# Kernel tuning notes

Measured on AMD Instinct MI355X. Metric: run time of the kernel, lower is better.

Reference implementation:

```python
import jax, jax.numpy as jnp
import numpy as np

N = 25000
E = 400000
MUL0 = 64   # multiplicity of 0e node irreps
MUL1 = 32   # multiplicity of 1o node irreps
NUM_BASIS = 10
FC_HIDDEN = 100
WEIGHT_NUMEL = 2 * MUL0 + 3 * MUL1  # 224: per-edge tp weights for the 5 uvu paths
MID_S = MUL0 + MUL1       # 96 mid scalar channels
MID_V = MUL0 + 2 * MUL1   # 128 mid vector channels
NUM_NEIGHBORS = 16.0


def setup_inputs() -> dict:
    key = jax.random.key(0)
    ks = jax.random.split(key, 16)
    inp = {
        'node_scalars': jax.random.normal(ks[0], (N, MUL0), jnp.float32),
        'node_vectors': jax.random.normal(ks[1], (N, MUL1, 3), jnp.float32),
        'node_attr': jnp.ones((N, 1), jnp.float32),
        'edge_src': jax.random.randint(ks[2], (E,), 0, N, jnp.int32),
        'edge_dst': jax.random.randint(ks[3], (E,), 0, N, jnp.int32),
        'edge_attr': jax.random.normal(ks[4], (E, 4), jnp.float32),
        'edge_scalars': jax.random.normal(ks[5], (E, NUM_BASIS), jnp.float32),
        # FullyConnectedNet: [10, 100, weight_numel], silu on hidden
        'W_fc1': jax.random.normal(ks[6], (NUM_BASIS, FC_HIDDEN), jnp.float32) / np.sqrt(NUM_BASIS),
        'W_fc2': jax.random.normal(ks[7], (FC_HIDDEN, WEIGHT_NUMEL), jnp.float32) / np.sqrt(FC_HIDDEN),
        # FullyConnectedTensorProduct with 0e attr == per-irrep linear mixing
        'W_sc_s': jax.random.normal(ks[8], (MUL0, MUL0), jnp.float32) / np.sqrt(MUL0),
        'W_sc_v': jax.random.normal(ks[9], (MUL1, MUL1), jnp.float32) / np.sqrt(MUL1),
        'W_l1_s': jax.random.normal(ks[10], (MUL0, MUL0), jnp.float32) / np.sqrt(MUL0),
        'W_l1_v': jax.random.normal(ks[11], (MUL1, MUL1), jnp.float32) / np.sqrt(MUL1),
        'W_l2_s': jax.random.normal(ks[12], (MID_S, MUL0), jnp.float32) / np.sqrt(MID_S),
        'W_l2_v': jax.random.normal(ks[13], (MID_V, MUL1), jnp.float32) / np.sqrt(MID_V),
        'W_l3': jax.random.normal(ks[14], (MID_S, 1), jnp.float32) / np.sqrt(MID_S),
    }
    return inp


def reference(node_scalars, node_vectors, node_attr, edge_src, edge_dst, edge_attr,
              edge_scalars, W_fc1, W_fc2, W_sc_s, W_sc_v, W_l1_s, W_l1_v,
              W_l2_s, W_l2_v, W_l3):
    n = node_scalars.shape[0]
    # --- edge-weight FC net: silu hidden, linear out -> per-edge tp weights ---
    w = jax.nn.silu(edge_scalars @ W_fc1) @ W_fc2  # [E, 224]
    w_00, w_01 = w[:, :MUL0], w[:, MUL0:2 * MUL0]                  # paths from 0e input
    w_10 = w[:, 2 * MUL0:2 * MUL0 + MUL1]                          # 1o x 0e -> 1o
    w_11s = w[:, 2 * MUL0 + MUL1:2 * MUL0 + 2 * MUL1]              # 1o x 1o -> 0e
    w_11v = w[:, 2 * MUL0 + 2 * MUL1:]                             # 1o x 1o -> 1o

    attr = node_attr  # [N,1] (0e attr => scalar multiplier)
    # self-connection and lin1 (per-irrep linear * attr)
    sc_s = (node_scalars @ W_sc_s) * attr
    sc_v = jnp.einsum('nuc,uv->nvc', node_vectors, W_sc_v) * attr[:, :, None]
    f_s = (node_scalars @ W_l1_s) * attr
    f_v = jnp.einsum('nuc,uv->nvc', node_vectors, W_l1_v) * attr[:, :, None]

    # --- gather source node features per edge ---
    s = f_s[edge_src]          # [E, MUL0]
    v = f_v[edge_src]          # [E, MUL1, 3]
    y0 = edge_attr[:, :1]      # l=0 sh
    y1 = edge_attr[:, 1:4]     # l=1 sh

    # --- weighted tensor product (uvu), CG-contracted paths ---
    mid_s = jnp.concatenate([
        w_00 * s * y0,                                              # 0e x 0e -> 0e
        w_11s * jnp.einsum('euc,ec->eu', v, y1) / jnp.sqrt(3.0),    # 1o x 1o -> 0e
    ], axis=1)                                                      # [E, 96]
    mid_v = jnp.concatenate([
        w_01[:, :, None] * s[:, :, None] * y1[:, None, :],          # 0e x 1o -> 1o
        w_10[:, :, None] * v * y0[:, :, None],                      # 1o x 0e -> 1o
        w_11v[:, :, None] * jnp.cross(v, y1[:, None, :]) / jnp.sqrt(2.0),  # 1o x 1o -> 1o
    ], axis=1)                                                      # [E, 128, 3]

    # --- scatter-add aggregation into destination nodes ---
    inv = 1.0 / jnp.sqrt(NUM_NEIGHBORS)
    agg_s = jax.ops.segment_sum(mid_s, edge_dst, num_segments=n) * inv
    agg_v = jax.ops.segment_sum(mid_v, edge_dst, num_segments=n) * inv

    # --- output linears and gated residual mix ---
    conv_s = (agg_s @ W_l2_s) * attr
    conv_v = jnp.einsum('nuc,uv->nvc', agg_v, W_l2_v) * attr[:, :, None]
    angle = 0.1 * (agg_s @ W_l3) * attr  # [N,1]
    cos, sin = jnp.cos(angle), jnp.sin(angle)  # sc output_mask is all-ones here
    out_s = cos * sc_s + sin * conv_s
    out_v = cos[:, :, None] * sc_v + sin[:, :, None] * conv_v
    return jnp.concatenate([out_s, out_v.reshape(n, -1)], axis=1)  # [N, 64+96]
```

## Files before the change

kernel.cpp:

```cpp
#include <hip/hip_runtime.h>

#define MUL0 64
#define MUL1 32
#define NBASIS 10
#define FCH 100
#define WNUMEL 224
#define MIDS 96
#define MIDV 128
#define EG 4

#define OFF_W1   0
#define OFF_W2   1000
#define OFF_WSCS 23400
#define OFF_WSCV 27496
#define OFF_WL1S 28520
#define OFF_WL1V 32616
#define OFF_WL2S 33640
#define OFF_WL2V 39784
#define OFF_WL3  43880
#define OFF_WEND 43976
#define OFF_FLAG 43980
#define OFF_W1FRAG 44032
#define OFF_W2FRAG 45824
#define OFF_DYN  60160

#define W1FRAG_N (112 * 32)
#define W2FRAG_N (4 * 224 * 32)

typedef __attribute__((ext_vector_type(8))) short short8;
typedef __attribute__((ext_vector_type(4))) float f32x4;

__device__ __forceinline__ float bf2f(unsigned short h) {
    unsigned int u = ((unsigned int)h) << 16;
    float f; __builtin_memcpy(&f, &u, 4); return f;
}
__device__ __forceinline__ unsigned short f2bf(float f) {
    unsigned int u; __builtin_memcpy(&u, &f, 4);
    u += 0x7fffu + ((u >> 16) & 1u);
    return (unsigned short)(u >> 16);
}
__device__ __forceinline__ float fast_silu(float x) {
    return x * __builtin_amdgcn_rcpf(1.0f + __expf(-x));
}
template<bool BF>
__device__ __forceinline__ float ldf(const void* p, size_t i) {
    if constexpr (BF) return bf2f(((const unsigned short*)p)[i]);
    else              return ((const float*)p)[i];
}
template<bool BF>
__device__ __forceinline__ void stf(void* p, size_t i, float v) {
    if constexpr (BF) ((unsigned short*)p)[i] = f2bf(v);
    else              ((float*)p)[i] = v;
}
template<bool BF>
__device__ __forceinline__ f32x4 ld4(const void* p, size_t i) {
    if constexpr (BF) {
        ushort4 h = *(const ushort4*)((const unsigned short*)p + i);
        return (f32x4){bf2f(h.x), bf2f(h.y), bf2f(h.z), bf2f(h.w)};
    } else {
        return *(const f32x4*)((const float*)p + i);
    }
}
__device__ __forceinline__ int wave_incl_scan(int v) {
    int lane = threadIdx.x & 63;
    #pragma unroll
    for (int d = 1; d < 64; d <<= 1) {
        int t = __shfl_up(v, d, 64);
        if (lane >= d) v += t;
    }
    return v;
}

template<bool BF>
__device__ __forceinline__ void node_pre_body(
    const void* __restrict__ ns, const void* __restrict__ nv,
    const void* __restrict__ attr,
    const void* __restrict__ Wl1s, const void* __restrict__ Wl1v,
    float* __restrict__ f_s, float* __restrict__ f_v, int i, int Nn)
{
    int stotal = Nn * MUL0;
    if (i < stotal) {
        int n = i >> 6, j = i & 63;
        float a = 0.f;
        #pragma unroll
        for (int u = 0; u < MUL0; u++)
            a = fmaf(ldf<BF>(ns, (size_t)n * MUL0 + u), ldf<BF>(Wl1s, u * MUL0 + j), a);
        f_s[i] = a * ldf<BF>(attr, n);
    } else {
        int m = i - stotal;
        if (m >= Nn * MUL1 * 3) return;
        int n = m / 96; int idx = m - n * 96;
        int vi = idx / 3; int c = idx - vi * 3;
        float a = 0.f;
        #pragma unroll
        for (int u = 0; u < MUL1; u++)
            a = fmaf(ldf<BF>(nv, (size_t)n * 96 + u * 3 + c), ldf<BF>(Wl1v, u * MUL1 + vi), a);
        f_v[m] = a * ldf<BF>(attr, n);
    }
}

__global__ __launch_bounds__(256) void k_prep(
    const void* __restrict__ ns, const void* __restrict__ nv,
    const void* __restrict__ attr,
    const void* __restrict__ a0, const void* __restrict__ a1,
    const void* __restrict__ a2, const void* __restrict__ a3,
    const void* __restrict__ a4, const void* __restrict__ a5,
    const void* __restrict__ a6, const void* __restrict__ a7,
    const void* __restrict__ a8,
    float* __restrict__ wsf,
    unsigned short* __restrict__ w1frag, unsigned short* __restrict__ w2frag,
    int* __restrict__ cnt, int* __restrict__ flag,
    float* __restrict__ f_s, float* __restrict__ f_v, int Nn)
{
    const bool bf = (((const unsigned int*)attr)[0] == 0x3F803F80u);
    int i = blockIdx.x * 256 + threadIdx.x;
    if (i == 0) *flag = bf ? 1 : 0;

    const int npre = Nn * 160;
    if (i < npre) {
        if (bf) node_pre_body<true >(ns, nv, attr, a4, a5, f_s, f_v, i, Nn);
        else    node_pre_body<false>(ns, nv, attr, a4, a5, f_s, f_v, i, Nn);
        return;
    }
    int m = i - npre;
    if (m < OFF_WEND) {
        const void* p; int off = m;
        if      (m < OFF_W2)   { p = a0; }
        else if (m < OFF_WSCS) { p = a1; off = m - OFF_W2; }
        else if (m < OFF_WSCV) { p = a2; off = m - OFF_WSCS; }
        else if (m < OFF_WL1S) { p = a3; off = m - OFF_WSCV; }
        else if (m < OFF_WL1V) { p = a4; off = m - OFF_WL1S; }
        else if (m < OFF_WL2S) { p = a5; off = m - OFF_WL1V; }
        else if (m < OFF_WL2V) { p = a6; off = m - OFF_WL2S; }
        else if (m < OFF_WL3)  { p = a7; off = m - OFF_WL2V; }
        else                   { p = a8; off = m - OFF_WL3; }
        wsf[m] = bf ? ldf<true>(p, off) : ldf<false>(p, off);
        return;
    }
    m -= OFF_WEND;
    if (m < W1FRAG_N) {
        int col = m >> 5, k = m & 31;
        float v = 0.f;
        if (col < FCH && k < NBASIS)
            v = bf ? ldf<true>(a0, k * FCH + col) : ldf<false>(a0, k * FCH + col);
        w1frag[m] = f2bf(v);
        return;
    }
    m -= W1FRAG_N;
    if (m < W2FRAG_N) {
        int q = m / (224 * 32); int r = m - q * 224 * 32;
        int n = r >> 5; int kk = r & 31;
        int k = q * 32 + kk;
        float v = 0.f;
        if (k < FCH)
            v = bf ? ldf<true>(a1, k * WNUMEL + n) : ldf<false>(a1, k * WNUMEL + n);
        w2frag[m] = f2bf(v);
        return;
    }
    m -= W2FRAG_N;
    if (m < Nn) cnt[m] = 0;
}

__global__ __launch_bounds__(256) void k_hist(
    const int* __restrict__ edst, int* __restrict__ cnt, int Ecnt)
{
    int e = blockIdx.x * 256 + threadIdx.x;
    if (e < Ecnt) atomicAdd(&cnt[edst[e]], 1);
}

__global__ __launch_bounds__(256) void k_scan_blk(
    const int* __restrict__ cnt, int* __restrict__ row_part,
    int* __restrict__ blk_sum, int Nn)
{
    __shared__ int ws4[4];
    int tid = threadIdx.x, lane = tid & 63, wid = tid >> 6;
    int i = blockIdx.x * 256 + tid;
    int v = (i < Nn) ? cnt[i] : 0;
    int incl = wave_incl_scan(v);
    if (lane == 63) ws4[wid] = incl;
    __syncthreads();
    int off = 0;
    #pragma unroll
    for (int w2 = 0; w2 < 4; w2++) off += (w2 < wid) ? ws4[w2] : 0;
    if (i < Nn) row_part[i] = off + incl - v;
    if (tid == 0) blk_sum[blockIdx.x] = ws4[0] + ws4[1] + ws4[2] + ws4[3];
}

__global__ __launch_bounds__(256) void k_scan_top(
    const int* __restrict__ blk_sum, int* __restrict__ blk_off,
    int* __restrict__ row_start, int NB, int Nn)
{
    __shared__ int ws4[4];
    int tid = threadIdx.x, lane = tid & 63, wid = tid >> 6;
    int v = (tid < NB) ? blk_sum[tid] : 0;
    int incl = wave_incl_scan(v);
    if (lane == 63) ws4[wid] = incl;
    __syncthreads();
    int off = 0;
    #pragma unroll
    for (int w2 = 0; w2 < 4; w2++) off += (w2 < wid) ? ws4[w2] : 0;
    if (tid < NB) blk_off[tid] = off + incl - v;
    if (tid == 0) row_start[Nn] = ws4[0] + ws4[1] + ws4[2] + ws4[3];
}

__global__ __launch_bounds__(256) void k_rowfix(
    const int* __restrict__ row_part, const int* __restrict__ blk_off,
    int* __restrict__ row_start, int* __restrict__ cur, int Nn)
{
    int i = blockIdx.x * 256 + threadIdx.x;
    if (i < Nn) { row_start[i] = blk_off[i >> 8] + row_part[i]; cur[i] = 0; }
}

__global__ __launch_bounds__(1024) void k_scan1(
    const int* __restrict__ cnt, int* __restrict__ row_start,
    int* __restrict__ cur, int Nn)
{
    __shared__ int wsum[16];
    __shared__ int s_off, s_tot;
    int tid = threadIdx.x, lane = tid & 63, wid = tid >> 6;
    if (tid == 0) s_off = 0;
    __syncthreads();
    for (int base = 0; base < Nn; base += 1024) {
        int i = base + tid;
        int v = (i < Nn) ? cnt[i] : 0;
        int incl = wave_incl_scan(v);
        if (lane == 63) wsum[wid] = incl;
        __syncthreads();
        if (wid == 0) {
            int wv = (lane < 16) ? wsum[lane] : 0;
            int wincl = wave_incl_scan(wv);
            if (lane < 16) wsum[lane] = wincl - wv;
            if (lane == 15) s_tot = wincl;
        }
        __syncthreads();
        int excl = s_off + wsum[wid] + incl - v;
        if (i < Nn) { row_start[i] = excl; cur[i] = 0; }
        __syncthreads();
        if (tid == 0) s_off += s_tot;
        __syncthreads();
    }
    if (threadIdx.x == 0) row_start[Nn] = s_off;
}

__global__ __launch_bounds__(256) void k_place(
    const int* __restrict__ edst, const int* __restrict__ esrc,
    const void* __restrict__ eattr,
    const int* __restrict__ row_start, int* __restrict__ cur,
    int* __restrict__ perm, int* __restrict__ srcs, float* __restrict__ y4,
    int Ecnt, const int* __restrict__ flag, int extras)
{
    int e = blockIdx.x * 256 + threadIdx.x;
    if (e >= Ecnt) return;
    int d = edst[e];
    int pos = row_start[d] + atomicAdd(&cur[d], 1);
    perm[pos] = e;
    if (extras) {
        srcs[pos] = esrc[e];
        float4 yv;
        if (*flag) {
            const unsigned short* ap = (const unsigned short*)eattr + (size_t)e * 4;
            yv = make_float4(bf2f(ap[0]), bf2f(ap[1]), bf2f(ap[2]), bf2f(ap[3]));
        } else {
            const float* ap = (const float*)eattr + (size_t)e * 4;
            yv = make_float4(ap[0], ap[1], ap[2], ap[3]);
        }
        ((float4*)y4)[pos] = yv;
    }
}

#define HFC_STRIDE 136
#define WS_STRIDE 232

__global__ __launch_bounds__(256) void k_fc(
    const void* __restrict__ escal, const int* __restrict__ perm,
    const unsigned short* __restrict__ w1frag, const unsigned short* __restrict__ w2frag,
    unsigned short* __restrict__ wbuf, int Ecnt, const int* __restrict__ flag)
{
    __shared__ __align__(16) unsigned short h_lds[64 * HFC_STRIDE];
    __shared__ __align__(16) unsigned short w_stage[64 * WS_STRIDE];
    const int tid  = threadIdx.x;
    const int lane = tid & 63;
    const int wave = tid >> 6;
    const int nl   = lane & 15;
    const int quad = lane >> 4;
    const int tb   = blockIdx.x * 64;

    for (int i = tid; i < 64 * 16; i += 256) {
        int row = i >> 4;
        h_lds[row * HFC_STRIDE + 112 + (i & 15)] = 0;
    }

    int eidx = tb + 16 * wave + nl;
    if (eidx >= Ecnt) eidx = Ecnt - 1;
    const int e = perm[eidx];
    short8 a = {0, 0, 0, 0, 0, 0, 0, 0};
    if (*flag) {
        const unsigned int* p = (const unsigned int*)((const unsigned short*)escal + (size_t)e * NBASIS);
        if (quad == 0) {
            unsigned int d0 = p[0], d1 = p[1], d2 = p[2], d3 = p[3];
            a = (short8){(short)d0, (short)(d0 >> 16), (short)d1, (short)(d1 >> 16),
                         (short)d2, (short)(d2 >> 16), (short)d3, (short)(d3 >> 16)};
        } else if (quad == 1) {
            unsigned int d4 = p[4];
            a = (short8){(short)d4, (short)(d4 >> 16), 0, 0, 0, 0, 0, 0};
        }
    } else {
        const float* p = (const float*)escal + (size_t)e * NBASIS;
        if (quad == 0) {
            a = (short8){(short)f2bf(p[0]), (short)f2bf(p[1]), (short)f2bf(p[2]), (short)f2bf(p[3]),
                         (short)f2bf(p[4]), (short)f2bf(p[5]), (short)f2bf(p[6]), (short)f2bf(p[7])};
        } else if (quad == 1) {
            a = (short8){(short)f2bf(p[8]), (short)f2bf(p[9]), 0, 0, 0, 0, 0, 0};
        }
    }

    {
        f32x4 hacc[7];
        #pragma unroll
        for (int t = 0; t < 7; t++) {
            short8 b = *(const short8*)&w1frag[(16 * t + nl) * 32 + quad * 8];
            hacc[t] = __builtin_amdgcn_mfma_f32_16x16x32_bf16(
                a, b, (f32x4){0.f, 0.f, 0.f, 0.f}, 0, 0, 0);
        }
        #pragma unroll
        for (int t = 0; t < 7; t++) {
            #pragma unroll
            for (int r = 0; r < 4; r++)
                h_lds[(16 * wave + quad * 4 + r) * HFC_STRIDE + 16 * t + nl] =
                    f2bf(fast_silu(hacc[t][r]));
        }
    }
    __syncthreads();

    #pragma unroll 2
    for (int t = 0; t < 14; t++) {
        f32x4 c = {0.f, 0.f, 0.f, 0.f};
        #pragma unroll
        for (int q = 0; q < 4; q++) {
            short8 av = *(const short8*)&h_lds[(16 * wave + nl) * HFC_STRIDE + q * 32 + quad * 8];
            short8 b = *(const short8*)&w2frag[((q * 224) + 16 * t + nl) * 32 + quad * 8];
            c = __builtin_amdgcn_mfma_f32_16x16x32_bf16(av, b, c, 0, 0, 0);
        }
        #pragma unroll
        for (int r = 0; r < 4; r++)
            w_stage[(16 * wave + quad * 4 + r) * WS_STRIDE + 16 * t + nl] = f2bf(c[r]);
    }
    __syncthreads();

    {
        unsigned short* wt = wbuf + (size_t)tb * WNUMEL;
        #pragma unroll
        for (int g = 0; g < 7; g++) {
            int m = g * 256 + tid;
            int row = m / 28, c8 = m - row * 28;
            uint4 v = *(const uint4*)&w_stage[row * WS_STRIDE + c8 * 8];
            *(uint4*)&wt[(size_t)m * 8] = v;
        }
    }
}

#define AGG_BODY(IDX, S)                                                     \
  {                                                                          \
    const int idx_ = (IDX);                                                  \
    const int srcn = srcs[idx_];                                             \
    const float4 y = ((const float4*)y4)[idx_];                              \
    const unsigned short* wrow = wbuf + (size_t)idx_ * WNUMEL;               \
    const float* fsr = f_s + (size_t)srcn * 64;                              \
    const float* fvr = f_v + (size_t)srcn * 96;                              \
    float fs_l = fsr[lane];                                                  \
    float v0 = fvr[lane2 * 3 + 0];                                           \
    float v1 = fvr[lane2 * 3 + 1];                                           \
    float v2 = fvr[lane2 * 3 + 2];                                           \
    float w00 = bf2f(wrow[lane]);                                            \
    float w01 = bf2f(wrow[64 + lane]);                                       \
    float wh  = bf2f(wrow[128 + lane]);                                      \
    float wx  = bf2f(wrow[160 + lane]);                                      \
    const float y0 = y.x, y1x = y.y, y1y = y.z, y1z = y.w;                   \
    acc0##S = fmaf(w00 * fs_l, y0 * k14, acc0##S);                           \
    float dot_ = v0 * y1x + v1 * y1y + v2 * y1z;                             \
    acc1##S = fmaf(wh * dot_, k13, acc1##S);                                 \
    float t1_ = w01 * fs_l * k14;                                            \
    accS0##S = fmaf(t1_, y1x, accS0##S);                                     \
    accS1##S = fmaf(t1_, y1y, accS1##S);                                     \
    accS2##S = fmaf(t1_, y1z, accS2##S);                                     \
    float cx_ = v1 * y1z - v2 * y1y;                                         \
    float cy_ = v2 * y1x - v0 * y1z;                                         \
    float cz_ = v0 * y1y - v1 * y1x;                                         \
    float e0_ = hi ? cx_ : v0;                                               \
    float e1_ = hi ? cy_ : v1;                                               \
    float e2_ = hi ? cz_ : v2;                                               \
    float tv_ = hi ? (wx * k12) : (wh * (y0 * k14));                         \
    accV0##S = fmaf(e0_, tv_, accV0##S);                                     \
    accV1##S = fmaf(e1_, tv_, accV1##S);                                     \
    accV2##S = fmaf(e2_, tv_, accV2##S);                                     \
  }

__global__ __launch_bounds__(256) void k_agg(
    const unsigned short* __restrict__ wbuf,
    const int* __restrict__ srcs, const float* __restrict__ y4,
    const int* __restrict__ row_start,
    const float* __restrict__ f_s, const float* __restrict__ f_v,
    const float* __restrict__ Wl3, const void* __restrict__ attr,
    float* __restrict__ agg_s, float* __restrict__ aggv,
    float* __restrict__ cosb, float* __restrict__ sinb,
    int Nn, const int* __restrict__ flag)
{
    const int tid  = threadIdx.x;
    const int lane = tid & 63;
    const int wave = tid >> 6;
    const int node = blockIdx.x * EG + wave;
    if (node >= Nn) return;

    const int lane2 = lane & 31;
    const bool hi = (lane >= 32);

    const int dlo = row_start[node];
    const int dhi = row_start[node + 1];
    const int mid = dlo + ((dhi - dlo) >> 1);

    const float k14 = 0.25f;
    const float k13 = 0.25f * 0.57735026918962576451f;
    const float k12 = 0.25f * 0.70710678118654752440f;

    float acc0A = 0.f, acc1A = 0.f, accS0A = 0.f, accS1A = 0.f, accS2A = 0.f;
    float accV0A = 0.f, accV1A = 0.f, accV2A = 0.f;
    float acc0B = 0.f, acc1B = 0.f, accS0B = 0.f, accS1B = 0.f, accS2B = 0.f;
    float accV0B = 0.f, accV1B = 0.f, accV2B = 0.f;

    int iA = dlo, iB = mid;
    for (; iA < mid; ++iA, ++iB) {
        AGG_BODY(iA, A);
        AGG_BODY(iB, B);
    }
    for (; iB < dhi; ++iB) {
        AGG_BODY(iB, B);
    }

    const float acc0  = acc0A + acc0B;
    const float acc1  = acc1A + acc1B;
    const float accS0 = accS0A + accS0B;
    const float accS1 = accS1A + accS1B;
    const float accS2 = accS2A + accS2B;
    const float accV0 = accV0A + accV0B;
    const float accV1 = accV1A + accV1B;
    const float accV2 = accV2A + accV2B;

    {
        float* as = agg_s + (size_t)node * MIDS;
        float* av = aggv  + (size_t)node * 384;
        as[lane] = acc0;
        if (hi) as[64 + lane2] = acc1;

        av[0 * 128 + lane] = accS0;
        av[1 * 128 + lane] = accS1;
        av[2 * 128 + lane] = accS2;
        const int vrow = hi ? (96 + lane2) : (64 + lane);
        av[0 * 128 + vrow] = accV0;
        av[1 * 128 + vrow] = accV1;
        av[2 * 128 + vrow] = accV2;

        float avv = acc0 * Wl3[lane];
        if (hi) avv = fmaf(acc1, Wl3[64 + lane2], avv);
        #pragma unroll
        for (int d = 1; d < 64; d <<= 1) avv += __shfl_xor(avv, d);
        if (lane == 0) {
            float at = (*flag) ? ldf<true>(attr, node) : ldf<false>(attr, node);
            float aa = 0.1f * avv * at;
            cosb[node] = __cosf(aa);
            sinb[node] = __sinf(aa);
        }
    }
}

#define WT_STRIDE 164

template<bool BF>
__device__ __forceinline__ void final_s_body(
    const float* __restrict__ agg_s, const void* __restrict__ ns,
    const float* __restrict__ cosb, const float* __restrict__ sinb,
    const void* __restrict__ attr, void* __restrict__ out,
    int Nn, const float* Wt, int lane, int nb)
{
    float acc_sc[8], acc_l2[8];
    int nidx[8];
    #pragma unroll
    for (int r = 0; r < 8; r++) {
        acc_sc[r] = 0.f; acc_l2[r] = 0.f;
        int n = nb + r; nidx[r] = (n < Nn) ? n : (Nn - 1);
    }
    #pragma unroll 2
    for (int t = 0; t < 16; t++) {
        f32x4 wv = *(const f32x4*)&Wt[lane * WT_STRIDE + 4 * t];
        #pragma unroll
        for (int r = 0; r < 8; r++) {
            f32x4 x = ld4<BF>(ns, (size_t)nidx[r] * 64 + 4 * t);
            acc_sc[r] = fmaf(x[0], wv[0], acc_sc[r]);
            acc_sc[r] = fmaf(x[1], wv[1], acc_sc[r]);
            acc_sc[r] = fmaf(x[2], wv[2], acc_sc[r]);
            acc_sc[r] = fmaf(x[3], wv[3], acc_sc[r]);
        }
    }
    #pragma unroll 2
    for (int t = 0; t < 24; t++) {
        f32x4 wv = *(const f32x4*)&Wt[lane * WT_STRIDE + 64 + 4 * t];
        #pragma unroll
        for (int r = 0; r < 8; r++) {
            f32x4 x = *(const f32x4*)(agg_s + (size_t)nidx[r] * 96 + 4 * t);
            acc_l2[r] = fmaf(x[0], wv[0], acc_l2[r]);
            acc_l2[r] = fmaf(x[1], wv[1], acc_l2[r]);
            acc_l2[r] = fmaf(x[2], wv[2], acc_l2[r]);
            acc_l2[r] = fmaf(x[3], wv[3], acc_l2[r]);
        }
    }
    #pragma unroll
    for (int r = 0; r < 8; r++) {
        int n = nb + r;
        if (n < Nn) {
            float cv = cosb[n], sv = sinb[n];
            float at = ldf<BF>(attr, n);
            stf<BF>(out, (size_t)n * 160 + lane, at * (cv * acc_sc[r] + sv * acc_l2[r]));
        }
    }
}

__global__ __launch_bounds__(256) void k_final_s(
    const float* __restrict__ agg_s, const void* __restrict__ ns,
    const float* __restrict__ Wscs, const float* __restrict__ Wl2s,
    const float* __restrict__ cosb, const float* __restrict__ sinb,
    const void* __restrict__ attr, void* __restrict__ out,
    int Nn, const int* __restrict__ flag)
{
    __shared__ float Wt[64 * WT_STRIDE];
    const int tid = threadIdx.x;
    for (int i = tid; i < 160 * 64; i += 256) {
        int u = i >> 6, j = i & 63;
        float w = (u < 64) ? Wscs[u * 64 + j] : Wl2s[(u - 64) * 64 + j];
        Wt[j * WT_STRIDE + u] = w;
    }
    __syncthreads();

    const int lane = tid & 63;
    const int wave = __builtin_amdgcn_readfirstlane(tid >> 6);
    const int nb   = (blockIdx.x * 4 + wave) * 8;
    if (nb >= Nn) return;
    if (*flag) final_s_body<true >(agg_s, ns, cosb, sinb, attr, out, Nn, Wt, lane, nb);
    else       final_s_body<false>(agg_s, ns, cosb, sinb, attr, out, Nn, Wt, lane, nb);
}

template<bool BF>
__device__ __forceinline__ void final_v_body(
    const float* __restrict__ aggv, const void* __restrict__ nv,
    const float* __restrict__ cosb, const float* __restrict__ sinb,
    const void* __restrict__ attr, void* __restrict__ out,
    int Nn, const float* Wt, int lane, int ub)
{
    const int vi   = lane & 31;
    const int grp  = lane >> 5;
    const int NU   = 3 * Nn;
    float acc_sc[8], acc_l2[8];
    int gidx[8], nn_[8], cc_[8];
    #pragma unroll
    for (int r = 0; r < 8; r++) {
        acc_sc[r] = 0.f; acc_l2[r] = 0.f;
        int g = ub + grp * 8 + r;
        if (g > NU - 1) g = NU - 1;
        gidx[r] = g;
        nn_[r] = (int)((unsigned)g / 3u);
        cc_[r] = g - 3 * nn_[r];
    }
    #pragma unroll 2
    for (int t = 0; t < 8; t++) {
        f32x4 wv = *(const f32x4*)&Wt[vi * WT_STRIDE + 4 * t];
        #pragma unroll
        for (int r = 0; r < 8; r++) {
            size_t b = (size_t)nn_[r] * 96 + (size_t)(4 * t) * 3 + cc_[r];
            float x0 = ldf<BF>(nv, b);
            float x1 = ldf<BF>(nv, b + 3);
            float x2 = ldf<BF>(nv, b + 6);
            float x3 = ldf<BF>(nv, b + 9);
            acc_sc[r] = fmaf(x0, wv[0], acc_sc[r]);
            acc_sc[r] = fmaf(x1, wv[1], acc_sc[r]);
            acc_sc[r] = fmaf(x2, wv[2], acc_sc[r]);
            acc_sc[r] = fmaf(x3, wv[3], acc_sc[r]);
        }
    }
    #pragma unroll 2
    for (int t = 0; t < 32; t++) {
        f32x4 wv = *(const f32x4*)&Wt[vi * WT_STRIDE + 32 + 4 * t];
        #pragma unroll
        for (int r = 0; r < 8; r++) {
            f32x4 x = *(const f32x4*)(aggv + (size_t)gidx[r] * 128 + 4 * t);
            acc_l2[r] = fmaf(x[0], wv[0], acc_l2[r]);
            acc_l2[r] = fmaf(x[1], wv[1], acc_l2[r]);
            acc_l2[r] = fmaf(x[2], wv[2], acc_l2[r]);
            acc_l2[r] = fmaf(x[3], wv[3], acc_l2[r]);
        }
    }
    #pragma unroll
    for (int r = 0; r < 8; r++) {
        int g = ub + grp * 8 + r;
        if (g < NU) {
            int n = nn_[r], c = cc_[r];
            float cv = cosb[n], sv = sinb[n];
            float at = ldf<BF>(attr, n);
            stf<BF>(out, (size_t)n * 160 + 64 + vi * 3 + c,
                    at * (cv * acc_sc[r] + sv * acc_l2[r]));
        }
    }
}

__global__ __launch_bounds__(256) void k_final_v(
    const float* __restrict__ aggv, const void* __restrict__ nv,
    const float* __restrict__ Wscv, const float* __restrict__ Wl2v,
    const float* __restrict__ cosb, const float* __restrict__ sinb,
    const void* __restrict__ attr, void* __restrict__ out,
    int Nn, const int* __restrict__ flag)
{
    __shared__ float Wt[32 * WT_STRIDE];
    const int tid = threadIdx.x;
    for (int i = tid; i < 160 * 32; i += 256) {
        int u = i >> 5, j = i & 31;
        float w = (u < 32) ? Wscv[u * 32 + j] : Wl2v[(u - 32) * 32 + j];
        Wt[j * WT_STRIDE + u] = w;
    }
    __syncthreads();

    const int lane = tid & 63;
    const int wave = __builtin_amdgcn_readfirstlane(tid >> 6);
    const int ub   = (blockIdx.x * 4 + wave) * 16;
    if (ub >= 3 * Nn) return;
    if (*flag) final_v_body<true >(aggv, nv, cosb, sinb, attr, out, Nn, Wt, lane, ub);
    else       final_v_body<false>(aggv, nv, cosb, sinb, attr, out, Nn, Wt, lane, ub);
}

#define ES_STRIDE 40
#define H_STRIDE 136
#define WL_STRIDE 225

__global__ __launch_bounds__(256) void k_edge_mfma(
    const void* __restrict__ escal, const void* __restrict__ eattr,
    const void* __restrict__ attr,
    const int* __restrict__ esrc,
    const int* __restrict__ row_start, const int* __restrict__ perm,
    const unsigned short* __restrict__ w1frag, const unsigned short* __restrict__ w2frag,
    const float* __restrict__ Wl3,
    const float* __restrict__ f_s, const float* __restrict__ f_v,
    float* __restrict__ agg_s, float* __restrict__ agg_v,
    float* __restrict__ cosb, float* __restrict__ sinb,
    int Nn, const int* __restrict__ flag)
{
    __shared__ __align__(16) unsigned short es_lds[64 * ES_STRIDE];
    __shared__ __align__(16) unsigned short h_lds[64 * H_STRIDE];
    __shared__ __align__(16) unsigned short w_lds[64 * WL_STRIDE];
    __shared__ float y_lds[64][4];
    __shared__ int   src_lds[64];

    const int tid  = threadIdx.x;
    const int lane = tid & 63;
    const int wave = tid >> 6;
    const int nl   = lane & 15;
    const int quad = lane >> 4;
    const int gbase = blockIdx.x * EG;
    const bool isbf = (*flag != 0);

    for (int i = tid; i < 64 * 22; i += 256) {
        int row = i / 22, k = 10 + (i - row * 22);
        es_lds[row * ES_STRIDE + k] = 0;
    }
    for (int i = tid; i < 64 * 16; i += 256) {
        int row = i >> 4, k = 112 + (i & 15);
        h_lds[row * H_STRIDE + k] = 0;
    }

    const int lane2 = lane & 31;
    const int u0 = lane / 3,  c0 = lane - 3 * u0;
    const int pB = 64 + lane;
    const int uB = pB / 3,    cB = pB - 3 * uB;
    const int p2 = 128 + lane;
    const int u2 = p2 / 3,    c2 = p2 - 3 * u2;
    const int pH = 64 + lane2;
    const int uH = pH / 3,    cH = pH - 3 * uH;
    const bool half = (lane < 32);

    const int node = gbase + wave;
    const int dlo = (node < Nn) ? row_start[node] : 0;
    const int dhi = (node < Nn) ? row_start[node + 1] : 0;

    float acc[9];
    #pragma unroll
    for (int s = 0; s < 9; s++) acc[s] = 0.f;

    const int gend    = (gbase + EG < Nn) ? (gbase + EG) : Nn;
    const int e_start = row_start[gbase];
    const int e_end   = row_start[gend];

    for (int tb = e_start; tb < e_end; tb += 64) {
        const int tcnt = (e_end - tb < 64) ? (e_end - tb) : 64;
        __syncthreads();

        {
            int i = tid & 63, part = tid >> 6;
            if (i < tcnt && part < 2) {
                int e = perm[tb + i];
                if (part == 0) {
                    unsigned int* dstp = (unsigned int*)&es_lds[i * ES_STRIDE];
                    if (isbf) {
                        const unsigned int* srcp =
                            (const unsigned int*)((const unsigned short*)escal + (size_t)e * NBASIS);
                        #pragma unroll
                        for (int t2 = 0; t2 < 5; t2++) dstp[t2] = srcp[t2];
                    } else {
                        const float* srcp = (const float*)escal + (size_t)e * NBASIS;
                        #pragma unroll
                        for (int t2 = 0; t2 < 5; t2++) {
                            unsigned int lo = f2bf(srcp[2 * t2]);
                            unsigned int hi = f2bf(srcp[2 * t2 + 1]);
                            dstp[t2] = lo | (hi << 16);
                        }
                    }
                } else {
                    src_lds[i] = esrc[e];
                    if (isbf) {
                        const unsigned short* ap = (const unsigned short*)eattr + (size_t)e * 4;
                        #pragma unroll
                        for (int t2 = 0; t2 < 4; t2++) y_lds[i][t2] = bf2f(ap[t2]);
                    } else {
                        const float* ap = (const float*)eattr + (size_t)e * 4;
                        #pragma unroll
                        for (int t2 = 0; t2 < 4; t2++) y_lds[i][t2] = ap[t2];
                    }
                }
            }
        }
        __syncthreads();

        {
            short8 a = *(const short8*)&es_lds[(16 * wave + nl) * ES_STRIDE + quad * 8];
            f32x4 hacc[7];
            #pragma unroll
            for (int t = 0; t < 7; t++) {
                short8 b = *(const short8*)&w1frag[(16 * t + nl) * 32 + quad * 8];
                hacc[t] = __builtin_amdgcn_mfma_f32_16x16x32_bf16(
                    a, b, (f32x4){0.f, 0.f, 0.f, 0.f}, 0, 0, 0);
            }
            #pragma unroll
            for (int t = 0; t < 7; t++) {
                #pragma unroll
                for (int r = 0; r < 4; r++)
                    h_lds[(16 * wave + quad * 4 + r) * H_STRIDE + 16 * t + nl] =
                        f2bf(fast_silu(hacc[t][r]));
            }
        }
        __syncthreads();

        #pragma unroll 2
        for (int t = 0; t < 14; t++) {
            f32x4 c = {0.f, 0.f, 0.f, 0.f};
            #pragma unroll
            for (int q = 0; q < 4; q++) {
                short8 a = *(const short8*)&h_lds[(16 * wave + nl) * H_STRIDE + q * 32 + quad * 8];
                short8 b = *(const short8*)&w2frag[((q * 224) + 16 * t + nl) * 32 + quad * 8];
                c = __builtin_amdgcn_mfma_f32_16x16x32_bf16(a, b, c, 0, 0, 0);
            }
            #pragma unroll
            for (int r = 0; r < 4; r++)
                w_lds[(16 * wave + quad * 4 + r) * WL_STRIDE + 16 * t + nl] = f2bf(c[r]);
        }
        __syncthreads();

        {
            int lo = dlo > tb ? dlo : tb;
            int hi = dhi < tb + tcnt ? dhi : tb + tcnt;
            for (int idx = lo; idx < hi; idx++) {
                const int i = idx - tb;
                const int srcn = src_lds[i];
                const float y0  = y_lds[i][0];
                const float y1x = y_lds[i][1];
                const float y1y = y_lds[i][2];
                const float y1z = y_lds[i][3];
                const float* fsr = f_s + (size_t)srcn * 64;
                const float* fvr = f_v + (size_t)srcn * 96;
                const unsigned short* wrow = &w_lds[i * WL_STRIDE];

                float fs_l  = fsr[lane];
                float fs_u0 = fsr[u0];
                float fs_uB = fsr[uB];
                float fs_u2 = fsr[u2];
                float fvA0 = fvr[lane2 * 3], fvA1 = fvr[lane2 * 3 + 1], fvA2 = fvr[lane2 * 3 + 2];
                float fvB0 = fvr[u0 * 3],    fvB1 = fvr[u0 * 3 + 1],    fvB2 = fvr[u0 * 3 + 2];
                float fvH0 = fvr[uH * 3],    fvH1 = fvr[uH * 3 + 1],    fvH2 = fvr[uH * 3 + 2];

                float y1c0 = (c0 == 0) ? y1x : (c0 == 1) ? y1y : y1z;
                float y1cB = (cB == 0) ? y1x : (cB == 1) ? y1y : y1z;
                float y1c2 = (c2 == 0) ? y1x : (c2 == 1) ? y1y : y1z;

                float w_s0 = bf2f(wrow[lane]);
                float w_s1 = bf2f(wrow[160 + lane2]);
                float w_s2 = bf2f(wrow[64 + u0]);
                float w_s3 = bf2f(wrow[64 + uB]);
                float w_s4 = bf2f(wrow[64 + u2]);
                float w_s5 = bf2f(wrow[128 + u0]);
                float w_s6 = bf2f(wrow[128 + uH]);
                float w_s7 = bf2f(wrow[192 + u0]);
                float w_s8 = bf2f(wrow[192 + uH]);

                const float k14 = 0.25f;
                const float k13 = 0.25f * 0.57735026918962576451f;
                const float k12 = 0.25f * 0.70710678118654752440f;

                acc[0] = fmaf(w_s0 * fs_l, y0 * k14, acc[0]);
                {
                    float dot = fvA0 * y1x + fvA1 * y1y + fvA2 * y1z;
                    acc[1] = fmaf(w_s1 * dot, k13, acc[1]);
                }
                acc[2] = fmaf(w_s2 * fs_u0, k14 * y1c0, acc[2]);
                acc[3] = fmaf(w_s3 * fs_uB, k14 * y1cB, acc[3]);
                acc[4] = fmaf(w_s4 * fs_u2, k14 * y1c2, acc[4]);
                {
                    float e5 = (c0 == 0) ? fvB0 : (c0 == 1) ? fvB1 : fvB2;
                    float e6 = (cH == 0) ? fvH0 : (cH == 1) ? fvH1 : fvH2;
                    acc[5] = fmaf(w_s5 * e5, k14 * y0, acc[5]);
                    acc[6] = fmaf(w_s6 * e6, k14 * y0, acc[6]);
                }
                {
                    float cr7 = (c0 == 0) ? (fvB1 * y1z - fvB2 * y1y)
                              : (c0 == 1) ? (fvB2 * y1x - fvB0 * y1z)
                                          : (fvB0 * y1y - fvB1 * y1x);
                    float cr8 = (cH == 0) ? (fvH1 * y1z - fvH2 * y1y)
                              : (cH == 1) ? (fvH2 * y1x - fvH0 * y1z)
                                          : (fvH0 * y1y - fvH1 * y1x);
                    acc[7] = fmaf(w_s7 * cr7, k12, acc[7]);
                    acc[8] = fmaf(w_s8 * cr8, k12, acc[8]);
                }
            }
        }
    }

    if (node < Nn) {
        float* as = agg_s + (size_t)node * MIDS;
        float* av = agg_v + (size_t)node * (MIDV * 3);
        as[lane] = acc[0];
        if (half) as[64 + lane] = acc[1];
        av[lane]       = acc[2];
        av[64 + lane]  = acc[3];
        av[128 + lane] = acc[4];
        av[192 + lane] = acc[5];
        if (half) av[256 + lane] = acc[6];
        av[288 + lane] = acc[7];
        if (half) av[352 + lane] = acc[8];

        float avv = acc[0] * Wl3[lane];
        if (half) avv = fmaf(acc[1], Wl3[64 + lane], avv);
        #pragma unroll
        for (int d = 1; d < 64; d <<= 1) avv += __shfl_xor(avv, d);
        if (lane == 0) {
            float at = isbf ? ldf<true>(attr, node) : ldf<false>(attr, node);
            float a = 0.1f * avv * at;
            cosb[node] = __cosf(a);
            sinb[node] = __sinf(a);
        }
    }
}

template<bool BF>
__device__ __forceinline__ void final_body(
    const void* __restrict__ ns, const void* __restrict__ nv,
    const void* __restrict__ attr,
    const float* __restrict__ Wscs, const float* __restrict__ Wscv,
    const float* __restrict__ Wl2s, const float* __restrict__ Wl2v,
    const float* __restrict__ agg_s, const float* __restrict__ agg_v,
    const float* __restrict__ cosb, const float* __restrict__ sinb,
    void* __restrict__ out, int Nn)
{
    int i = blockIdx.x * 256 + threadIdx.x;
    int stotal = Nn * MUL0;
    if (i < stotal) {
        int n = i >> 6, j = i & 63;
        const float* ar = agg_s + (size_t)n * MIDS;
        float a1 = 0.f, a2 = 0.f;
        #pragma unroll
        for (int u = 0; u < MUL0; u++)
            a1 = fmaf(ldf<BF>(ns, (size_t)n * MUL0 + u), Wscs[u * MUL0 + j], a1);
        #pragma unroll
        for (int u = 0; u < MIDS; u++) a2 = fmaf(ar[u], Wl2s[u * MUL0 + j], a2);
        float o = ldf<BF>(attr, n) * (cosb[n] * a1 + sinb[n] * a2);
        stf<BF>(out, (size_t)n * 160 + j, o);
    } else {
        int m = i - stotal;
        if (m >= Nn * 96) return;
        int n = m / 96; int idx = m - n * 96;
        int vi = idx / 3; int c = idx - vi * 3;
        const float* ar = agg_v + (size_t)n * (MIDV * 3);
        float a1 = 0.f, a2 = 0.f;
        #pragma unroll
        for (int u = 0; u < MUL1; u++)
            a1 = fmaf(ldf<BF>(nv, (size_t)n * 96 + u * 3 + c), Wscv[u * MUL1 + vi], a1);
        #pragma unroll
        for (int u = 0; u < MIDV; u++) a2 = fmaf(ar[u * 3 + c], Wl2v[u * MUL1 + vi], a2);
        float o = ldf<BF>(attr, n) * (cosb[n] * a1 + sinb[n] * a2);
        stf<BF>(out, (size_t)n * 160 + 64 + idx, o);
    }
}
__global__ __launch_bounds__(256) void k_final(
    const void* ns, const void* nv, const void* attr,
    const float* Wscs, const float* Wscv,
    const float* Wl2s, const float* Wl2v,
    const float* agg_s, const float* agg_v,
    const float* cosb, const float* sinb,
    void* out, int Nn, const int* flag)
{
    if (*flag) final_body<true >(ns, nv, attr, Wscs, Wscv, Wl2s, Wl2v, agg_s, agg_v, cosb, sinb, out, Nn);
    else       final_body<false>(ns, nv, attr, Wscs, Wscv, Wl2s, Wl2v, agg_s, agg_v, cosb, sinb, out, Nn);
}

extern "C" void kernel_launch(void* const* d_in, const int* in_sizes, int n_in,
                              void* d_out, int out_size, void* d_ws, size_t ws_size,
                              hipStream_t stream)
{
    const void* ns    = d_in[0];
    const void* nv    = d_in[1];
    const void* attr  = d_in[2];
    const int*  esrc  = (const int*)d_in[3];
    const int*  edst  = (const int*)d_in[4];
    const void* eattr = d_in[5];
    const void* escal = d_in[6];

    const int Nn   = in_sizes[2];
    const int Ecnt = in_sizes[3];

    float* ws = (float*)d_ws;
    int* flag = (int*)(ws + OFF_FLAG);
    unsigned short* w1frag = (unsigned short*)(ws + OFF_W1FRAG);
    unsigned short* w2frag = (unsigned short*)(ws + OFF_W2FRAG);

    size_t o = OFF_DYN;
    const size_t OFF_FS   = o; o += (size_t)Nn * 64;
    const size_t OFF_FV   = o; o += (size_t)Nn * 96;
    const size_t OFF_AGGS = o; o += (size_t)Nn * 96;
    const size_t OFF_AGGV = o; o += (size_t)Nn * 384;
    const size_t OFF_COS  = o; o += Nn;
    const size_t OFF_SIN  = o; o += Nn;
    const size_t OFF_CNT  = o; o += Nn;
    const size_t OFF_ROW  = o; o += Nn + 1;
    const size_t OFF_CUR  = o; o += Nn;
    const size_t OFF_RPART= o; o += Nn;
    const size_t OFF_BSUM = o; o += 256;
    const size_t OFF_BOFF = o; o += 256;
    const size_t OFF_PERM = o; o += Ecnt;
    const size_t OFF_SRCS = o; o += Ecnt;
    o = (o + 3) & ~(size_t)3;
    const size_t OFF_Y4   = o; o += (size_t)Ecnt * 4;
    o = (o + 15) & ~(size_t)15;
    const size_t OFF_WBUF = o;
    const int tiles = (Ecnt + 63) / 64;
    o += (size_t)tiles * 64 * 112;
    const size_t need_bytes = o * sizeof(float);

    int* cnt       = (int*)(ws + OFF_CNT);
    int* row_start = (int*)(ws + OFF_ROW);
    int* cur       = (int*)(ws + OFF_CUR);
    int* row_part  = (int*)(ws + OFF_RPART);
    int* blk_sum   = (int*)(ws + OFF_BSUM);
    int* blk_off   = (int*)(ws + OFF_BOFF);
    int* perm      = (int*)(ws + OFF_PERM);
    int* srcs      = (int*)(ws + OFF_SRCS);
    float* y4      = ws + OFF_Y4;
    unsigned short* wbuf = (unsigned short*)(ws + OFF_WBUF);

    const int NB = (Nn + 255) / 256;
    const bool split = (ws_size >= need_bytes) && (NB <= 256);

    const int prep_work = Nn * 160 + OFF_WEND + W1FRAG_N + W2FRAG_N + Nn;
    k_prep<<<(prep_work + 255) / 256, 256, 0, stream>>>(
        ns, nv, attr,
        d_in[7], d_in[8], d_in[9], d_in[10], d_in[11], d_in[12],
        d_in[13], d_in[14], d_in[15],
        ws, w1frag, w2frag, cnt, flag,
        ws + OFF_FS, ws + OFF_FV, Nn);

    k_hist<<<(Ecnt + 255) / 256, 256, 0, stream>>>(edst, cnt, Ecnt);

    if (split) {
        k_scan_blk<<<NB, 256, 0, stream>>>(cnt, row_part, blk_sum, Nn);
        k_scan_top<<<1, 256, 0, stream>>>(blk_sum, blk_off, row_start, NB, Nn);
        k_rowfix<<<NB, 256, 0, stream>>>(row_part, blk_off, row_start, cur, Nn);
        k_place<<<(Ecnt + 255) / 256, 256, 0, stream>>>(
            edst, esrc, eattr, row_start, cur, perm, srcs, y4, Ecnt, flag, 1);

        k_fc<<<tiles, 256, 0, stream>>>(escal, perm, w1frag, w2frag, wbuf, Ecnt, flag);

        k_agg<<<(Nn + EG - 1) / EG, 256, 0, stream>>>(
            wbuf, srcs, y4, row_start,
            ws + OFF_FS, ws + OFF_FV, ws + OFF_WL3, attr,
            ws + OFF_AGGS, ws + OFF_AGGV, ws + OFF_COS, ws + OFF_SIN,
            Nn, flag);

        k_final_s<<<(Nn + 31) / 32, 256, 0, stream>>>(
            ws + OFF_AGGS, ns, ws + OFF_WSCS, ws + OFF_WL2S,
            ws + OFF_COS, ws + OFF_SIN, attr, (void*)d_out, Nn, flag);
        k_final_v<<<(3 * Nn + 63) / 64, 256, 0, stream>>>(
            ws + OFF_AGGV, nv, ws + OFF_WSCV, ws + OFF_WL2V,
            ws + OFF_COS, ws + OFF_SIN, attr, (void*)d_out, Nn, flag);
    } else {
        k_scan1<<<1, 1024, 0, stream>>>(cnt, row_start, cur, Nn);
        k_place<<<(Ecnt + 255) / 256, 256, 0, stream>>>(
            edst, esrc, eattr, row_start, cur, perm, srcs, y4, Ecnt, flag, 0);
        k_edge_mfma<<<(Nn + EG - 1) / EG, 256, 0, stream>>>(
            escal, eattr, attr, esrc, row_start, perm, w1frag, w2frag,
            ws + OFF_WL3,
            ws + OFF_FS, ws + OFF_FV,
            ws + OFF_AGGS, ws + OFF_AGGV, ws + OFF_COS, ws + OFF_SIN,
            Nn, flag);
        k_final<<<((Nn * 160) + 255) / 256, 256, 0, stream>>>(
            ns, nv, attr,
            ws + OFF_WSCS, ws + OFF_WSCV, ws + OFF_WL2S, ws + OFF_WL2V,
            ws + OFF_AGGS, ws + OFF_AGGV, ws + OFF_COS, ws + OFF_SIN,
            (void*)d_out, Nn, flag);
    }
}
```

Before: 535.6 us.

## Split FC2 output columns across waves and write bf16 weights directly

The second FC layer is re-partitioned so each wave owns a slice of output column tiles across all 64 edges, instead of each wave owning 16 edges across all 14 column tiles. Each w2frag B fragment is now loaded once per wave and reused for four edge groups, which cuts global/L2 traffic for the weight matrix. The LDS staging buffer and its extra barrier are removed, and results go straight to global memory. In exchange, the stores become scattered 2-byte writes instead of coalesced 16-byte writes, and the work is split unevenly (4/4/3/3 tiles per wave).

```diff
diff --git a/kernel.cpp b/kernel.cpp
--- a/kernel.cpp
+++ b/kernel.cpp
@@ -269,7 +269,6 @@
 }
 
 #define HFC_STRIDE 136
-#define WS_STRIDE 232
 
 __global__ __launch_bounds__(256) void k_fc(
     const void* __restrict__ escal, const int* __restrict__ perm,
@@ -277,7 +276,6 @@
     unsigned short* __restrict__ wbuf, int Ecnt, const int* __restrict__ flag)
 {
     __shared__ __align__(16) unsigned short h_lds[64 * HFC_STRIDE];
-    __shared__ __align__(16) unsigned short w_stage[64 * WS_STRIDE];
     const int tid  = threadIdx.x;
     const int lane = tid & 63;
     const int wave = tid >> 6;
@@ -332,29 +330,31 @@
     }
     __syncthreads();
 
-    #pragma unroll 2
-    for (int t = 0; t < 14; t++) {
-        f32x4 c = {0.f, 0.f, 0.f, 0.f};
-        #pragma unroll
-        for (int q = 0; q < 4; q++) {
-            short8 av = *(const short8*)&h_lds[(16 * wave + nl) * HFC_STRIDE + q * 32 + quad * 8];
-            short8 b = *(const short8*)&w2frag[((q * 224) + 16 * t + nl) * 32 + quad * 8];
-            c = __builtin_amdgcn_mfma_f32_16x16x32_bf16(av, b, c, 0, 0, 0);
-        }
-        #pragma unroll
-        for (int r = 0; r < 4; r++)
-            w_stage[(16 * wave + quad * 4 + r) * WS_STRIDE + 16 * t + nl] = f2bf(c[r]);
-    }
-    __syncthreads();
-
     {
-        unsigned short* wt = wbuf + (size_t)tb * WNUMEL;
-        #pragma unroll
-        for (int g = 0; g < 7; g++) {
-            int m = g * 256 + tid;
-            int row = m / 28, c8 = m - row * 28;
-            uint4 v = *(const uint4*)&w_stage[row * WS_STRIDE + c8 * 8];
-            *(uint4*)&wt[(size_t)m * 8] = v;
+        const int tsta = (wave < 2) ? wave * 4 : 8 + (wave - 2) * 3;
+        const int tend = (wave < 2) ? tsta + 4 : tsta + 3;
+        for (int t = tsta; t < tend; t++) {
+            short8 b0 = *(const short8*)&w2frag[(0 * 224 + 16 * t + nl) * 32 + quad * 8];
+            short8 b1 = *(const short8*)&w2frag[(1 * 224 + 16 * t + nl) * 32 + quad * 8];
+            short8 b2 = *(const short8*)&w2frag[(2 * 224 + 16 * t + nl) * 32 + quad * 8];
+            short8 b3 = *(const short8*)&w2frag[(3 * 224 + 16 * t + nl) * 32 + quad * 8];
+            #pragma unroll
+            for (int eg = 0; eg < 4; eg++) {
+                const unsigned short* hrow = &h_lds[(16 * eg + nl) * HFC_STRIDE];
+                f32x4 c = {0.f, 0.f, 0.f, 0.f};
+                c = __builtin_amdgcn_mfma_f32_16x16x32_bf16(
+                    *(const short8*)&hrow[0 * 32 + quad * 8], b0, c, 0, 0, 0);
+                c = __builtin_amdgcn_mfma_f32_16x16x32_bf16(
+                    *(const short8*)&hrow[1 * 32 + quad * 8], b1, c, 0, 0, 0);
+                c = __builtin_amdgcn_mfma_f32_16x16x32_bf16(
+                    *(const short8*)&hrow[2 * 32 + quad * 8], b2, c, 0, 0, 0);
+                c = __builtin_amdgcn_mfma_f32_16x16x32_bf16(
+                    *(const short8*)&hrow[3 * 32 + quad * 8], b3, c, 0, 0, 0);
+                #pragma unroll
+                for (int r = 0; r < 4; r++)
+                    wbuf[(size_t)(tb + 16 * eg + quad * 4 + r) * WNUMEL + 16 * t + nl] =
+                        f2bf(c[r]);
+            }
         }
     }
 }
```

New measurement: 500.8 us. -6.5%, faster.
